# Optimization experiments

Measured on AMD Instinct MI355X. Metric: run time of the kernel, lower is better.

## Reference

```python
import jax, jax.numpy as jnp
import numpy as np

GROUPS = 32
EPS = 1e-5


def group_norm(x, scale, bias):
    # x: [B, C, T]
    b, c, t = x.shape
    xg = x.reshape(b, GROUPS, c // GROUPS, t)
    mean = xg.mean(axis=(2, 3), keepdims=True)
    var = xg.var(axis=(2, 3), keepdims=True)
    xg = (xg - mean) * jax.lax.rsqrt(var + EPS)
    return xg.reshape(b, c, t) * scale[None, :, None] + bias[None, :, None]


def setup_inputs() -> dict:
    key = jax.random.key(0)
    ks = jax.random.split(key, 7)
    B, C, H, W = 8, 512, 32, 32
    x = jax.random.normal(ks[0], (B, C, H, W), dtype=jnp.float32)
    gn_scale = jnp.ones((C,), jnp.float32)
    gn_bias = jnp.zeros((C,), jnp.float32)
    qkv_w = jax.random.normal(ks[1], (3 * C, C), jnp.float32) / np.sqrt(C)
    qkv_b = jnp.zeros((3 * C,), jnp.float32)
    # proj_out is zero-initialized in the original; use small random weights
    # so the attention path contributes to the output (trained-model behavior).
    proj_w = jax.random.normal(ks[2], (C, C), jnp.float32) / np.sqrt(C)
    proj_b = jnp.zeros((C,), jnp.float32)
    return {"x": x, "gn_scale": gn_scale, "gn_bias": gn_bias,
            "qkv_w": qkv_w, "qkv_b": qkv_b, "proj_w": proj_w, "proj_b": proj_b}


def reference(x, gn_scale, gn_bias, qkv_w, qkv_b, proj_w, proj_b):
    NUM_HEADS = 8
    b, c, *spatial = x.shape
    t = int(np.prod(spatial))
    xf = x.reshape(b, c, t)                                   # [B,C,T]
    xn = group_norm(xf, gn_scale, gn_bias)
    qkv = jnp.einsum('oc,bct->bot', qkv_w, xn) + qkv_b[None, :, None]  # [B,3C,T]
    # legacy layout: reshape to heads BEFORE splitting into q,k,v thirds
    qkv = qkv.reshape(b * NUM_HEADS, -1, t)                   # [B*H, 3C/H, T]
    ch = qkv.shape[1] // 3
    q, k, v = jnp.split(qkv, 3, axis=1)                       # each [B*H, ch, T]
    scale = 1.0 / np.sqrt(np.sqrt(ch))
    w = jnp.einsum('bct,bcs->bts', q * scale, k * scale)      # [B*H, T, T]
    w = jax.nn.softmax(w.astype(jnp.float32), axis=-1).astype(w.dtype)
    h = jnp.einsum('bts,bcs->bct', w, v)                      # [B*H, ch, T]
    h = h.reshape(b, c, t)
    h = jnp.einsum('oc,bct->bot', proj_w, h) + proj_b[None, :, None]
    return (xf + h).reshape(b, c, *spatial)
```

## Files before the change

### kernel.cpp

```cpp
#include <hip/hip_runtime.h>

typedef __bf16 bf16;
typedef __attribute__((ext_vector_type(8))) __bf16 bf16x8;
typedef __attribute__((ext_vector_type(4))) __bf16 bf16x4;
typedef __attribute__((ext_vector_type(4))) float f32x4;

#define MFMA(a, b, c) __builtin_amdgcn_mfma_f32_16x16x32_bf16(a, b, c, 0, 0, 0)
#define GLOAD_LDS(g, l)                                                        \
  __builtin_amdgcn_global_load_lds(                                            \
      (const __attribute__((address_space(1))) void*)(g),                      \
      (__attribute__((address_space(3))) void*)(l), 16, 0, 0)

#if __has_builtin(__builtin_amdgcn_exp2f)
#define EXP2(x) __builtin_amdgcn_exp2f(x)
#else
#define EXP2(x) exp2f(x)
#endif

#define C1LOG 0.18033688011f

__device__ __forceinline__ int swz64(int row, int col) {
  return row * 64 + (col ^ ((row & 7) << 3));
}

__global__ __launch_bounds__(256, 2) void k_pre(
    const float* __restrict__ x, const float* __restrict__ gs,
    const float* __restrict__ gb, const float* __restrict__ qw,
    const float* __restrict__ pw, bf16* __restrict__ xnT,
    bf16* __restrict__ wq, bf16* __restrict__ wp) {
  int tid = threadIdx.x;
  if (blockIdx.x >= 256) {
    int i = (blockIdx.x - 256) * 256 + tid;
    int idx = i * 4;
    float4 v;
    bf16* o;
    if (idx < 786432) {
      v = *(const float4*)(qw + idx);
      o = wq + idx;
    } else {
      int j = idx - 786432;
      v = *(const float4*)(pw + j);
      o = wp + j;
    }
    o[0] = (bf16)v.x; o[1] = (bf16)v.y; o[2] = (bf16)v.z; o[3] = (bf16)v.w;
    return;
  }
  __shared__ float xs[16 * 1024];
  __shared__ float red[2][4];
  int blk = blockIdx.x;
  int b = blk >> 5, g = blk & 31;
  const float* xp = x + ((size_t)(b * 512 + g * 16)) * 1024;
  float s = 0.f, ss = 0.f;
  for (int i = tid; i < 4096; i += 256) {
    float4 v = ((const float4*)xp)[i];
    *(float4*)&xs[i * 4] = v;
    s += v.x + v.y + v.z + v.w;
    ss += v.x * v.x + v.y * v.y + v.z * v.z + v.w * v.w;
  }
#pragma unroll
  for (int m = 1; m < 64; m <<= 1) {
    s += __shfl_xor(s, m);
    ss += __shfl_xor(ss, m);
  }
  int wid = tid >> 6;
  if ((tid & 63) == 0) { red[0][wid] = s; red[1][wid] = ss; }
  __syncthreads();
  float fs = red[0][0] + red[0][1] + red[0][2] + red[0][3];
  float fss = red[1][0] + red[1][1] + red[1][2] + red[1][3];
  float mean = fs * (1.f / 16384.f);
  float var = fss * (1.f / 16384.f) - mean * mean;
  float inv = rsqrtf(var + 1e-5f);
  float a_[16], b_[16];
#pragma unroll
  for (int cl = 0; cl < 16; ++cl) {
    float sc = gs[g * 16 + cl] * inv;
    a_[cl] = sc;
    b_[cl] = gb[g * 16 + cl] - mean * sc;
  }
  int t0 = tid * 4;
  bf16 tmp[4][16];
#pragma unroll
  for (int cl = 0; cl < 16; ++cl) {
    float4 v = *(float4*)&xs[cl * 1024 + t0];
    tmp[0][cl] = (bf16)(v.x * a_[cl] + b_[cl]);
    tmp[1][cl] = (bf16)(v.y * a_[cl] + b_[cl]);
    tmp[2][cl] = (bf16)(v.z * a_[cl] + b_[cl]);
    tmp[3][cl] = (bf16)(v.w * a_[cl] + b_[cl]);
  }
  bf16* outp = xnT + (size_t)b * 1024 * 512 + g * 16;
#pragma unroll
  for (int k = 0; k < 4; ++k) {
    *(bf16x8*)(outp + (size_t)(t0 + k) * 512) = *(bf16x8*)&tmp[k][0];
    *(bf16x8*)(outp + (size_t)(t0 + k) * 512 + 8) = *(bf16x8*)&tmp[k][8];
  }
}

__global__ void k_qkv(const bf16* __restrict__ xnT, const bf16* __restrict__ wq,
                      const float* __restrict__ qb, bf16* __restrict__ qkvT,
                      bf16* __restrict__ vTout) {
  int bid = blockIdx.x;
  int swz = (bid & 7) * 96 + (bid >> 3);
  int nt = swz % 12, mt = swz / 12;
  int tid = threadIdx.x, lane = tid & 63;
  int wid = tid >> 6, wr = wid >> 1, wc = wid & 1;
  int lr = lane & 15, lk8 = (lane >> 4) * 8, prow4 = (lane >> 4) * 4;
  __shared__ __align__(16) bf16 lA[8192], lB[8192];
  const bf16* Ab = xnT + (size_t)mt * 128 * 512;
  const bf16* Bb = wq + (size_t)nt * 128 * 512;
  f32x4 acc[4][4] = {};
  int ubase = tid & 192;
  for (int kt = 0; kt < 8; ++kt) {
    __syncthreads();
#pragma unroll
    for (int i = 0; i < 4; ++i) {
      int s = i * 256 + tid;
      int r = s >> 3, cc = (s & 7) ^ (r & 7);
      GLOAD_LDS(Ab + (size_t)r * 512 + kt * 64 + cc * 8, lA + (i * 256 + ubase) * 8);
      GLOAD_LDS(Bb + (size_t)r * 512 + kt * 64 + cc * 8, lB + (i * 256 + ubase) * 8);
    }
    __syncthreads();
#pragma unroll
    for (int ksl = 0; ksl < 2; ++ksl) {
      bf16x8 aF[4], bF[4];
#pragma unroll
      for (int m = 0; m < 4; ++m)
        aF[m] = *(bf16x8*)&lA[swz64(wr * 64 + m * 16 + lr, ksl * 32 + lk8)];
#pragma unroll
      for (int n = 0; n < 4; ++n)
        bF[n] = *(bf16x8*)&lB[swz64(wc * 64 + n * 16 + lr, ksl * 32 + lk8)];
      __builtin_amdgcn_s_setprio(1);
#pragma unroll
      for (int m = 0; m < 4; ++m)
#pragma unroll
        for (int n = 0; n < 4; ++n) acc[m][n] = MFMA(aF[m], bF[n], acc[m][n]);
      __builtin_amdgcn_s_setprio(0);
    }
  }
#pragma unroll
  for (int n = 0; n < 4; ++n) {
    int o = nt * 128 + wc * 64 + n * 16 + lr;
    float bias = qb[o];
    int hh = o / 192;
    int om = o - hh * 192;
    bool isv = om >= 128;
    float scl = (om >= 64 && om < 128) ? C1LOG : 1.0f;
    int c = om - 128;
#pragma unroll
    for (int m = 0; m < 4; ++m) {
      int row0 = mt * 128 + wr * 64 + m * 16 + prow4;
      if (isv) {
        int bb = row0 >> 10, t0 = row0 & 1023;
        bf16x4 v4;
#pragma unroll
        for (int r = 0; r < 4; ++r) v4[r] = (bf16)(acc[m][n][r] + bias);
        *(bf16x4*)&vTout[(((size_t)bb * 8 + hh) * 64 + c) * 1024 + t0] = v4;
      } else {
#pragma unroll
        for (int r = 0; r < 4; ++r)
          qkvT[(size_t)(row0 + r) * 1536 + o] = (bf16)((acc[m][n][r] + bias) * scl);
      }
    }
  }
}

__global__ __launch_bounds__(512, 4) void k_attn(const bf16* __restrict__ qkvT,
                                                 const bf16* __restrict__ vT,
                                                 bf16* __restrict__ hT) {
  int d = blockIdx.x;
  int head = (d & 7) * 8 + (d >> 6);
  int qt = (d >> 3) & 7;
  int b = head >> 3, hh = head & 7;
  int tid = threadIdx.x, lane = tid & 63, wid = tid >> 6;
  int lr = lane & 15, hi = lane >> 4, lk8 = hi * 8;

  __shared__ __align__(16) bf16 KT[3][4096];
  __shared__ __align__(16) bf16 VTl[3][4096];
  __shared__ __align__(16) bf16 PT[8][1024];

  const bf16* qbase = qkvT + (size_t)b * 1024 * 1536 + hh * 192;
  const bf16* kbase = qbase + 64;
  const bf16* vbase = vT + (size_t)head * 64 * 1024;

  int tq = qt * 128 + wid * 16 + lr;
  bf16x8 qf0 = *(const bf16x8*)(qbase + (size_t)tq * 1536 + lk8);
  bf16x8 qf1 = *(const bf16x8*)(qbase + (size_t)tq * 1536 + 32 + lk8);

  f32x4 hacc[4] = {};
  float m2 = -1e30f, l_ = 0.f;

  int r_ = tid >> 3;
  int cc_ = (tid & 7) ^ (r_ & 7);
  const bf16* ksrc = kbase + (size_t)r_ * 1536 + cc_ * 8;
  const bf16* vsrc = vbase + (size_t)r_ * 1024 + cc_ * 8;
  int lbase = (tid >> 6) * 512;

  GLOAD_LDS(ksrc, KT[0] + lbase);
  GLOAD_LDS(vsrc, VTl[0] + lbase);
  GLOAD_LDS(ksrc + (size_t)64 * 1536, KT[1] + lbase);
  GLOAD_LDS(vsrc + 64, VTl[1] + lbase);

  for (int it = 0; it < 16; ++it) {
    int cur = it % 3;
    if (it < 15)
      asm volatile("s_waitcnt vmcnt(2)" ::: "memory");
    else
      asm volatile("s_waitcnt vmcnt(0)" ::: "memory");
    __builtin_amdgcn_s_barrier();
    __builtin_amdgcn_sched_barrier(0);
    if (it < 14) {
      int sb = (it + 2) * 64;
      int nx = (it + 2) % 3;
      GLOAD_LDS(ksrc + (size_t)sb * 1536, KT[nx] + lbase);
      GLOAD_LDS(vsrc + sb, VTl[nx] + lbase);
    }
    f32x4 sc[4];
#pragma unroll
    for (int n = 0; n < 4; ++n) sc[n] = f32x4{0.f, 0.f, 0.f, 0.f};
    __builtin_amdgcn_s_setprio(1);
#pragma unroll
    for (int n = 0; n < 4; ++n) {
      bf16x8 kA0 = *(bf16x8*)&KT[cur][swz64(n * 16 + lr, lk8)];
      bf16x8 kA1 = *(bf16x8*)&KT[cur][swz64(n * 16 + lr, 32 + lk8)];
      sc[n] = MFMA(kA0, qf0, sc[n]);
      sc[n] = MFMA(kA1, qf1, sc[n]);
    }
    __builtin_amdgcn_s_setprio(0);
    float tm = fmaxf(
        fmaxf(fmaxf(fmaxf(sc[0][0], sc[0][1]), fmaxf(sc[0][2], sc[0][3])),
              fmaxf(fmaxf(sc[1][0], sc[1][1]), fmaxf(sc[1][2], sc[1][3]))),
        fmaxf(fmaxf(fmaxf(sc[2][0], sc[2][1]), fmaxf(sc[2][2], sc[2][3])),
              fmaxf(fmaxf(sc[3][0], sc[3][1]), fmaxf(sc[3][2], sc[3][3]))));
    tm = fmaxf(tm, __shfl_xor(tm, 16));
    tm = fmaxf(tm, __shfl_xor(tm, 32));
    if (__any(tm > m2 + 7.213f)) {
      float mn = fmaxf(m2, tm);
      float al = EXP2(m2 - mn);
      m2 = mn;
      l_ *= al;
#pragma unroll
      for (int n = 0; n < 4; ++n) {
        hacc[n][0] *= al; hacc[n][1] *= al; hacc[n][2] *= al; hacc[n][3] *= al;
      }
    }
    float rs = 0.f;
#pragma unroll
    for (int n = 0; n < 4; ++n) {
      float e0 = EXP2(sc[n][0] - m2), e1 = EXP2(sc[n][1] - m2);
      float e2 = EXP2(sc[n][2] - m2), e3 = EXP2(sc[n][3] - m2);
      rs += (e0 + e1) + (e2 + e3);
      bf16x4 p4;
      p4[0] = (bf16)e0; p4[1] = (bf16)e1; p4[2] = (bf16)e2; p4[3] = (bf16)e3;
      *(bf16x4*)&PT[wid][swz64(lr, n * 16 + hi * 4)] = p4;
    }
    rs += __shfl_xor(rs, 16);
    rs += __shfl_xor(rs, 32);
    l_ += rs;
    asm volatile("s_waitcnt lgkmcnt(0)" ::: "memory");
    __builtin_amdgcn_sched_barrier(0);
    bf16x8 pa0 = *(bf16x8*)&PT[wid][swz64(lr, lk8)];
    bf16x8 pa1 = *(bf16x8*)&PT[wid][swz64(lr, 32 + lk8)];
    __builtin_amdgcn_s_setprio(1);
#pragma unroll
    for (int n = 0; n < 4; ++n) {
      bf16x8 vA0 = *(bf16x8*)&VTl[cur][swz64(n * 16 + lr, lk8)];
      bf16x8 vA1 = *(bf16x8*)&VTl[cur][swz64(n * 16 + lr, 32 + lk8)];
      hacc[n] = MFMA(vA0, pa0, hacc[n]);
      hacc[n] = MFMA(vA1, pa1, hacc[n]);
    }
    __builtin_amdgcn_s_setprio(0);
  }
  float invl = 1.f / l_;
  bf16* dst = hT + ((size_t)b * 1024 + tq) * 512 + hh * 64 + hi * 4;
#pragma unroll
  for (int n = 0; n < 4; ++n) {
    bf16x4 o4;
#pragma unroll
    for (int r = 0; r < 4; ++r) o4[r] = (bf16)(hacc[n][r] * invl);
    *(bf16x4*)(dst + n * 16) = o4;
  }
}

__global__ void k_proj(const bf16* __restrict__ hT, const bf16* __restrict__ wp,
                       const float* __restrict__ pb, const float* __restrict__ x,
                       float* __restrict__ out) {
  int bid = blockIdx.x;
  int swz = (bid & 7) * 64 + (bid >> 3);
  int nt = swz & 7, mt = swz >> 3;
  int tid = threadIdx.x, lane = tid & 63;
  int wid = tid >> 6, wr = wid >> 1, wc = wid & 1;
  int lr = lane & 15, lk8 = (lane >> 4) * 8, prow4 = (lane >> 4) * 4;
  __shared__ __align__(16) bf16 lA[8192], lB[4096];
  const bf16* Ab = hT + (size_t)mt * 128 * 512;
  const bf16* Bb = wp + (size_t)nt * 64 * 512;
  f32x4 acc[4][2] = {};
  int ubase = tid & 192;
  for (int kt = 0; kt < 8; ++kt) {
    __syncthreads();
#pragma unroll
    for (int i = 0; i < 4; ++i) {
      int s = i * 256 + tid;
      int r = s >> 3, cc = (s & 7) ^ (r & 7);
      GLOAD_LDS(Ab + (size_t)r * 512 + kt * 64 + cc * 8, lA + (i * 256 + ubase) * 8);
    }
#pragma unroll
    for (int i = 0; i < 2; ++i) {
      int s = i * 256 + tid;
      int r = s >> 3, cc = (s & 7) ^ (r & 7);
      GLOAD_LDS(Bb + (size_t)r * 512 + kt * 64 + cc * 8, lB + (i * 256 + ubase) * 8);
    }
    __syncthreads();
#pragma unroll
    for (int ksl = 0; ksl < 2; ++ksl) {
      bf16x8 aF[4], bF[2];
#pragma unroll
      for (int m = 0; m < 4; ++m)
        aF[m] = *(bf16x8*)&lA[swz64(wr * 64 + m * 16 + lr, ksl * 32 + lk8)];
#pragma unroll
      for (int n = 0; n < 2; ++n)
        bF[n] = *(bf16x8*)&lB[swz64(wc * 32 + n * 16 + lr, ksl * 32 + lk8)];
      __builtin_amdgcn_s_setprio(1);
#pragma unroll
      for (int m = 0; m < 4; ++m)
#pragma unroll
        for (int n = 0; n < 2; ++n) acc[m][n] = MFMA(aF[m], bF[n], acc[m][n]);
      __builtin_amdgcn_s_setprio(0);
    }
  }
#pragma unroll
  for (int n = 0; n < 2; ++n) {
    int o = nt * 64 + wc * 32 + n * 16 + lr;
    float bias = pb[o];
#pragma unroll
    for (int m = 0; m < 4; ++m) {
      int row0 = mt * 128 + wr * 64 + m * 16 + prow4;
      int bb = row0 >> 10, t0 = row0 & 1023;
      size_t off = ((size_t)bb * 512 + o) * 1024 + t0;
      float4 xv = *(const float4*)(x + off);
      float4 rr;
      rr.x = acc[m][n][0] + xv.x + bias;
      rr.y = acc[m][n][1] + xv.y + bias;
      rr.z = acc[m][n][2] + xv.z + bias;
      rr.w = acc[m][n][3] + xv.w + bias;
      *(float4*)(out + off) = rr;
    }
  }
}

extern "C" void kernel_launch(void* const* d_in, const int* in_sizes, int n_in,
                              void* d_out, int out_size, void* d_ws, size_t ws_size,
                              hipStream_t stream) {
  const float* x = (const float*)d_in[0];
  const float* gs = (const float*)d_in[1];
  const float* gb = (const float*)d_in[2];
  const float* qw = (const float*)d_in[3];
  const float* qb = (const float*)d_in[4];
  const float* pw = (const float*)d_in[5];
  const float* pb = (const float*)d_in[6];
  float* out = (float*)d_out;
  char* ws = (char*)d_ws;
  bf16* xnT  = (bf16*)(ws);
  bf16* qkvT = (bf16*)(ws + 8388608);
  bf16* vT   = (bf16*)(ws + 33554432);
  bf16* hT   = (bf16*)(ws + 41943040);
  bf16* wq   = (bf16*)(ws + 50331648);
  bf16* wp   = (bf16*)(ws + 51904512);

  k_pre<<<1280, 256, 0, stream>>>(x, gs, gb, qw, pw, xnT, wq, wp);
  k_qkv<<<768, 256, 0, stream>>>(xnT, wq, qb, qkvT, vT);
  k_attn<<<512, 512, 0, stream>>>(qkvT, vT, hT);
  k_proj<<<512, 256, 0, stream>>>(hT, wp, pb, x, out);
}
```

Before: 76.82 us.

## Double-buffer 128-key attention tiles and compute row sums with MFMA

The attention kernel now processes 128 keys per iteration in two 8192-element double buffers, replacing the previous triple-buffered 64-key tiles. This halves the barrier and rescale-check count per row but waits for all outstanding loads (vmcnt(0)) each iteration, so less load latency is hidden. The softmax denominator is accumulated with an extra MFMA against a ones vector instead of VALU adds and cross-lane shuffles. Working registers for the eight score tiles go up, and the sum now uses the bf16-rounded probabilities, so it matches the numerator rounding rather than the fp32 values.

```diff
diff --git a/kernel.cpp b/kernel.cpp
--- a/kernel.cpp
+++ b/kernel.cpp
@@ -173,8 +173,8 @@
   int tid = threadIdx.x, lane = tid & 63, wid = tid >> 6;
   int lr = lane & 15, hi = lane >> 4, lk8 = hi * 8;
 
-  __shared__ __align__(16) bf16 KT[3][4096];
-  __shared__ __align__(16) bf16 VTl[3][4096];
+  __shared__ __align__(16) bf16 KT[2][8192];
+  __shared__ __align__(16) bf16 VTl[2][8192];
   __shared__ __align__(16) bf16 PT[8][1024];
 
   const bf16* qbase = qkvT + (size_t)b * 1024 * 1536 + hh * 192;
@@ -186,90 +186,103 @@
   bf16x8 qf1 = *(const bf16x8*)(qbase + (size_t)tq * 1536 + 32 + lk8);
 
   f32x4 hacc[4] = {};
-  float m2 = -1e30f, l_ = 0.f;
-
-  int r_ = tid >> 3;
-  int cc_ = (tid & 7) ^ (r_ & 7);
-  const bf16* ksrc = kbase + (size_t)r_ * 1536 + cc_ * 8;
-  const bf16* vsrc = vbase + (size_t)r_ * 1024 + cc_ * 8;
-  int lbase = (tid >> 6) * 512;
-
-  GLOAD_LDS(ksrc, KT[0] + lbase);
-  GLOAD_LDS(vsrc, VTl[0] + lbase);
-  GLOAD_LDS(ksrc + (size_t)64 * 1536, KT[1] + lbase);
-  GLOAD_LDS(vsrc + 64, VTl[1] + lbase);
-
-  for (int it = 0; it < 16; ++it) {
-    int cur = it % 3;
-    if (it < 15)
-      asm volatile("s_waitcnt vmcnt(2)" ::: "memory");
-    else
-      asm volatile("s_waitcnt vmcnt(0)" ::: "memory");
+  f32x4 lsum = {};
+  float m2 = -1e30f;
+
+  int rr8 = tid >> 3;
+  int cc_ = (tid & 7) ^ (rr8 & 7);
+  const bf16* ksrcT = kbase + (size_t)rr8 * 1536 + cc_ * 8;
+  const bf16* vsrcT = vbase + (size_t)rr8 * 1024 + cc_ * 8;
+  int ldst = wid * 512;
+
+  bf16x8 ones;
+#pragma unroll
+  for (int j = 0; j < 8; ++j) ones[j] = (bf16)1.0f;
+
+  GLOAD_LDS(ksrcT, KT[0] + ldst);
+  GLOAD_LDS(ksrcT + (size_t)64 * 1536, KT[0] + 4096 + ldst);
+  GLOAD_LDS(vsrcT, VTl[0] + ldst);
+  GLOAD_LDS(vsrcT + 64, VTl[0] + 4096 + ldst);
+
+  for (int it = 0; it < 8; ++it) {
+    int cur = it & 1;
+    asm volatile("s_waitcnt vmcnt(0)" ::: "memory");
     __builtin_amdgcn_s_barrier();
     __builtin_amdgcn_sched_barrier(0);
-    if (it < 14) {
-      int sb = (it + 2) * 64;
-      int nx = (it + 2) % 3;
-      GLOAD_LDS(ksrc + (size_t)sb * 1536, KT[nx] + lbase);
-      GLOAD_LDS(vsrc + sb, VTl[nx] + lbase);
-    }
-    f32x4 sc[4];
-#pragma unroll
-    for (int n = 0; n < 4; ++n) sc[n] = f32x4{0.f, 0.f, 0.f, 0.f};
+    if (it < 7) {
+      size_t sb = (size_t)(it + 1) * 128;
+      const bf16* kp = ksrcT + sb * 1536;
+      const bf16* vp = vsrcT + sb;
+      GLOAD_LDS(kp, KT[cur ^ 1] + ldst);
+      GLOAD_LDS(kp + (size_t)64 * 1536, KT[cur ^ 1] + 4096 + ldst);
+      GLOAD_LDS(vp, VTl[cur ^ 1] + ldst);
+      GLOAD_LDS(vp + 64, VTl[cur ^ 1] + 4096 + ldst);
+    }
+    f32x4 sc[8];
+#pragma unroll
+    for (int n = 0; n < 8; ++n) sc[n] = f32x4{0.f, 0.f, 0.f, 0.f};
     __builtin_amdgcn_s_setprio(1);
 #pragma unroll
-    for (int n = 0; n < 4; ++n) {
+    for (int n = 0; n < 8; ++n) {
       bf16x8 kA0 = *(bf16x8*)&KT[cur][swz64(n * 16 + lr, lk8)];
       bf16x8 kA1 = *(bf16x8*)&KT[cur][swz64(n * 16 + lr, 32 + lk8)];
       sc[n] = MFMA(kA0, qf0, sc[n]);
       sc[n] = MFMA(kA1, qf1, sc[n]);
     }
     __builtin_amdgcn_s_setprio(0);
-    float tm = fmaxf(
-        fmaxf(fmaxf(fmaxf(sc[0][0], sc[0][1]), fmaxf(sc[0][2], sc[0][3])),
-              fmaxf(fmaxf(sc[1][0], sc[1][1]), fmaxf(sc[1][2], sc[1][3]))),
-        fmaxf(fmaxf(fmaxf(sc[2][0], sc[2][1]), fmaxf(sc[2][2], sc[2][3])),
-              fmaxf(fmaxf(sc[3][0], sc[3][1]), fmaxf(sc[3][2], sc[3][3]))));
+    float a0 = fmaxf(fmaxf(sc[0][0], sc[0][1]), fmaxf(sc[0][2], sc[0][3]));
+    float a1 = fmaxf(fmaxf(sc[1][0], sc[1][1]), fmaxf(sc[1][2], sc[1][3]));
+    float a2 = fmaxf(fmaxf(sc[2][0], sc[2][1]), fmaxf(sc[2][2], sc[2][3]));
+    float a3 = fmaxf(fmaxf(sc[3][0], sc[3][1]), fmaxf(sc[3][2], sc[3][3]));
+    float a4 = fmaxf(fmaxf(sc[4][0], sc[4][1]), fmaxf(sc[4][2], sc[4][3]));
+    float a5 = fmaxf(fmaxf(sc[5][0], sc[5][1]), fmaxf(sc[5][2], sc[5][3]));
+    float a6 = fmaxf(fmaxf(sc[6][0], sc[6][1]), fmaxf(sc[6][2], sc[6][3]));
+    float a7 = fmaxf(fmaxf(sc[7][0], sc[7][1]), fmaxf(sc[7][2], sc[7][3]));
+    float tm = fmaxf(fmaxf(fmaxf(a0, a1), fmaxf(a2, a3)),
+                     fmaxf(fmaxf(a4, a5), fmaxf(a6, a7)));
     tm = fmaxf(tm, __shfl_xor(tm, 16));
     tm = fmaxf(tm, __shfl_xor(tm, 32));
     if (__any(tm > m2 + 7.213f)) {
       float mn = fmaxf(m2, tm);
       float al = EXP2(m2 - mn);
       m2 = mn;
-      l_ *= al;
+      lsum[0] *= al; lsum[1] *= al; lsum[2] *= al; lsum[3] *= al;
 #pragma unroll
       for (int n = 0; n < 4; ++n) {
         hacc[n][0] *= al; hacc[n][1] *= al; hacc[n][2] *= al; hacc[n][3] *= al;
       }
     }
-    float rs = 0.f;
-#pragma unroll
-    for (int n = 0; n < 4; ++n) {
-      float e0 = EXP2(sc[n][0] - m2), e1 = EXP2(sc[n][1] - m2);
-      float e2 = EXP2(sc[n][2] - m2), e3 = EXP2(sc[n][3] - m2);
-      rs += (e0 + e1) + (e2 + e3);
-      bf16x4 p4;
-      p4[0] = (bf16)e0; p4[1] = (bf16)e1; p4[2] = (bf16)e2; p4[3] = (bf16)e3;
-      *(bf16x4*)&PT[wid][swz64(lr, n * 16 + hi * 4)] = p4;
-    }
-    rs += __shfl_xor(rs, 16);
-    rs += __shfl_xor(rs, 32);
-    l_ += rs;
-    asm volatile("s_waitcnt lgkmcnt(0)" ::: "memory");
-    __builtin_amdgcn_sched_barrier(0);
-    bf16x8 pa0 = *(bf16x8*)&PT[wid][swz64(lr, lk8)];
-    bf16x8 pa1 = *(bf16x8*)&PT[wid][swz64(lr, 32 + lk8)];
-    __builtin_amdgcn_s_setprio(1);
-#pragma unroll
-    for (int n = 0; n < 4; ++n) {
-      bf16x8 vA0 = *(bf16x8*)&VTl[cur][swz64(n * 16 + lr, lk8)];
-      bf16x8 vA1 = *(bf16x8*)&VTl[cur][swz64(n * 16 + lr, 32 + lk8)];
-      hacc[n] = MFMA(vA0, pa0, hacc[n]);
-      hacc[n] = MFMA(vA1, pa1, hacc[n]);
-    }
-    __builtin_amdgcn_s_setprio(0);
-  }
-  float invl = 1.f / l_;
+#pragma unroll
+    for (int h = 0; h < 2; ++h) {
+#pragma unroll
+      for (int n4 = 0; n4 < 4; ++n4) {
+        int n = 4 * h + n4;
+        bf16x4 p4;
+        p4[0] = (bf16)EXP2(sc[n][0] - m2);
+        p4[1] = (bf16)EXP2(sc[n][1] - m2);
+        p4[2] = (bf16)EXP2(sc[n][2] - m2);
+        p4[3] = (bf16)EXP2(sc[n][3] - m2);
+        *(bf16x4*)&PT[wid][swz64(lr, n4 * 16 + hi * 4)] = p4;
+      }
+      asm volatile("s_waitcnt lgkmcnt(0)" ::: "memory");
+      __builtin_amdgcn_sched_barrier(0);
+      bf16x8 pa0 = *(bf16x8*)&PT[wid][swz64(lr, lk8)];
+      bf16x8 pa1 = *(bf16x8*)&PT[wid][swz64(lr, 32 + lk8)];
+      const bf16* vb = VTl[cur] + h * 4096;
+      __builtin_amdgcn_s_setprio(1);
+#pragma unroll
+      for (int n4 = 0; n4 < 4; ++n4) {
+        bf16x8 vA0 = *(bf16x8*)&vb[swz64(n4 * 16 + lr, lk8)];
+        bf16x8 vA1 = *(bf16x8*)&vb[swz64(n4 * 16 + lr, 32 + lk8)];
+        hacc[n4] = MFMA(vA0, pa0, hacc[n4]);
+        hacc[n4] = MFMA(vA1, pa1, hacc[n4]);
+      }
+      lsum = MFMA(ones, pa0, lsum);
+      lsum = MFMA(ones, pa1, lsum);
+      __builtin_amdgcn_s_setprio(0);
+    }
+  }
+  float invl = 1.f / lsum[0];
   bf16* dst = hT + ((size_t)b * 1024 + tq) * 512 + hh * 64 + hi * 4;
 #pragma unroll
   for (int n = 0; n < 4; ++n) {
```

Result: faster. 74.09 us (median of 2 runs) (-3.6%).
